# Kernel optimization log

Measured on AMD Instinct MI355X. Metric: run time of the kernel, lower is better.

## Reference

```python
import jax, jax.numpy as jnp
import numpy as np

B, S, D, H, DFF = 4, 2048, 1024, 16, 4096
DK = D // H
EPS = 1e-6


def layernorm(x, w, b):
    # Faithful to source: unbiased std (ddof=1), divides by (std + eps).
    mean = jnp.mean(x, axis=-1, keepdims=True)
    std = jnp.std(x, axis=-1, keepdims=True, ddof=1)
    return w * (x - mean) / (std + EPS) + b


def setup_inputs() -> dict:
    key = jax.random.key(0)
    ks = jax.random.split(key, 16)
    g = lambda k, shape: (jax.random.normal(k, shape, dtype=jnp.float32) * 0.02)
    inp = {
        "x": jax.random.normal(ks[0], (B, S, D), dtype=jnp.float32),
        "mask": jnp.ones((B, 1, 1, S), dtype=jnp.int32),
        # attention projections (stored [in, out]; math identical to torch Linear)
        "wq": g(ks[1], (D, D)), "bq": jnp.zeros((D,), jnp.float32),
        "wk": g(ks[2], (D, D)), "bk": jnp.zeros((D,), jnp.float32),
        "wv": g(ks[3], (D, D)), "bv": jnp.zeros((D,), jnp.float32),
        "wo": g(ks[4], (D, D)), "bo": jnp.zeros((D,), jnp.float32),
        # feed-forward
        "w1": g(ks[5], (D, DFF)), "b1": jnp.zeros((DFF,), jnp.float32),
        "w2": g(ks[6], (DFF, D)), "b2": jnp.zeros((D,), jnp.float32),
        # layer norms
        "ln1_w": jnp.ones((D,), jnp.float32), "ln1_b": jnp.zeros((D,), jnp.float32),
        "ln2_w": jnp.ones((D,), jnp.float32), "ln2_b": jnp.zeros((D,), jnp.float32),
    }
    return inp


def attention(xn, mask, wq, bq, wk, bk, wv, bv, wo, bo):
    q = (xn @ wq + bq).reshape(B, S, H, DK)
    k = (xn @ wk + bk).reshape(B, S, H, DK)
    v = (xn @ wv + bv).reshape(B, S, H, DK)
    scores = jnp.einsum("bqhd,bkhd->bhqk", q, k) / jnp.sqrt(jnp.float32(DK))
    scores = jnp.where(mask == 0, -jnp.inf, scores)
    attn = jax.nn.softmax(scores, axis=-1)  # dropout identity at inference
    out = jnp.einsum("bhqk,bkhd->bqhd", attn, v).reshape(B, S, D)
    return out @ wo + bo


def reference(x, mask, wq, bq, wk, bk, wv, bv, wo, bo,
              w1, b1, w2, b2, ln1_w, ln1_b, ln2_w, ln2_b):
    # pre-norm residual 1: self-attention
    x = x + attention(layernorm(x, ln1_w, ln1_b), mask,
                      wq, bq, wk, bk, wv, bv, wo, bo)
    # pre-norm residual 2: FFN
    xn = layernorm(x, ln2_w, ln2_b)
    ffn = jax.nn.relu(xn @ w1 + b1) @ w2 + b2
    return x + ffn
```

## Files before the change

kernel.cpp:

```cpp
#include <hip/hip_runtime.h>


typedef unsigned short u16;
typedef unsigned u32;
typedef __bf16 bf16x8 __attribute__((ext_vector_type(8)));
typedef float f32x4 __attribute__((ext_vector_type(4)));
typedef float f32x16 __attribute__((ext_vector_type(16)));

typedef __attribute__((address_space(1))) const void* as1_cvp;
typedef __attribute__((address_space(3))) void* as3_vp;

__device__ __forceinline__ void async_copy16(const void* g, void* l) {
  __builtin_amdgcn_global_load_lds((as1_cvp)g, (as3_vp)l, 16, 0, 0);
}

__device__ __forceinline__ u16 f2bf(float f) {
  unsigned u = __float_as_uint(f);
  u += 0x7fffu + ((u >> 16) & 1u);
  return (u16)(u >> 16);
}

__device__ __forceinline__ float fast_exp2(float x) {
  return __builtin_amdgcn_exp2f(x);
}

__device__ __forceinline__ u32 cvt_pk_bf16(float lo, float hi) {
  u32 d;
  asm("v_cvt_pk_bf16_f32 %0, %1, %2" : "=v"(d) : "v"(lo), "v"(hi));
  return d;
}

__device__ __forceinline__ void permlane32_swap(u32& x, u32& y) {
  asm volatile("v_permlane32_swap_b32 %0, %1" : "+v"(x), "+v"(y));
}

__global__ __launch_bounds__(256) void k_transpose_bf16(
    const float* __restrict__ src, u16* __restrict__ dst, int K, int N,
    float scale) {
  __shared__ float tile[32][33];
  int n0 = blockIdx.x * 32, k0 = blockIdx.y * 32;
  int c = threadIdx.x & 31, r0 = threadIdx.x >> 5;
#pragma unroll
  for (int i = 0; i < 32; i += 8)
    tile[r0 + i][c] = src[(size_t)(k0 + r0 + i) * N + n0 + c];
  __syncthreads();
#pragma unroll
  for (int i = 0; i < 32; i += 8)
    dst[(size_t)(n0 + r0 + i) * K + k0 + c] = f2bf(tile[c][r0 + i] * scale);
}

__global__ __launch_bounds__(256) void k_pack_bias(
    const float* __restrict__ bq, const float* __restrict__ bk,
    const float* __restrict__ bv, float* __restrict__ out, float qscale) {
  int i = blockIdx.x * 256 + threadIdx.x;
  float v;
  if (i < 1024) v = bq[i] * qscale;
  else if (i < 2048) v = bk[i - 1024];
  else v = bv[i - 2048];
  out[i] = v;
}

__global__ __launch_bounds__(256) void k_maskadd(
    const int* __restrict__ mask, float* __restrict__ madd) {
  int i = blockIdx.x * 256 + threadIdx.x;
  madd[i] = mask[i] ? 0.0f : -1e30f;
}

__global__ __launch_bounds__(256) void k_layernorm_bf16(
    const float* __restrict__ x, const float* __restrict__ w,
    const float* __restrict__ b, u16* __restrict__ out) {
  const int D = 1024;
  int row = blockIdx.x, tid = threadIdx.x;
  const float4* xr = (const float4*)(x + (size_t)row * D);
  float4 v = xr[tid];
  float s = v.x + v.y + v.z + v.w;
  float ss = v.x * v.x + v.y * v.y + v.z * v.z + v.w * v.w;
#pragma unroll
  for (int off = 1; off < 64; off <<= 1) {
    s += __shfl_xor(s, off);
    ss += __shfl_xor(ss, off);
  }
  __shared__ float rs[4], rss[4];
  int wave = tid >> 6, lane = tid & 63;
  if (lane == 0) { rs[wave] = s; rss[wave] = ss; }
  __syncthreads();
  float S_ = rs[0] + rs[1] + rs[2] + rs[3];
  float SS = rss[0] + rss[1] + rss[2] + rss[3];
  float mean = S_ * (1.0f / D);
  float var = (SS - (float)D * mean * mean) * (1.0f / (D - 1));
  float inv = 1.0f / (sqrtf(fmaxf(var, 0.0f)) + 1e-6f);
  float4 wv = ((const float4*)w)[tid], bv = ((const float4*)b)[tid];
  u16* orow = out + (size_t)row * D + tid * 4;
  orow[0] = f2bf(wv.x * (v.x - mean) * inv + bv.x);
  orow[1] = f2bf(wv.y * (v.y - mean) * inv + bv.y);
  orow[2] = f2bf(wv.z * (v.z - mean) * inv + bv.z);
  orow[3] = f2bf(wv.w * (v.w - mean) * inv + bv.w);
}

template <bool RELU, bool HAS_RES, bool OUT_BF16>
__global__ __launch_bounds__(512, 2) void k_gemm2(
    const u16* __restrict__ A, const u16* __restrict__ Bt,
    const float* __restrict__ bias, const float* __restrict__ res,
    void* __restrict__ outp, int M, int N, int K) {
  __shared__ __align__(16) u16 lds[3 * 24576];
  const int tid = threadIdx.x;
  const int lane = tid & 63, wave = tid >> 6;
  const int quad = lane >> 4, l16 = lane & 15;
  const int m0 = blockIdx.x * 256, n0 = blockIdx.y * 128;
  const int wm = (wave >> 1) * 64, wn = (wave & 1) * 64;

  const int srow = tid >> 3;
  const int schunk8 = ((tid & 7) ^ (srow & 7)) * 8;
  const u16* gA0 = A + (size_t)(m0 + srow) * K + schunk8;
  const u16* gA1 = A + (size_t)(m0 + 64 + srow) * K + schunk8;
  const u16* gA2 = A + (size_t)(m0 + 128 + srow) * K + schunk8;
  const u16* gA3 = A + (size_t)(m0 + 192 + srow) * K + schunk8;
  const u16* gB0 = Bt + (size_t)(n0 + srow) * K + schunk8;
  const u16* gB1 = Bt + (size_t)(n0 + 64 + srow) * K + schunk8;

  auto STAGE = [&](int t, int s) {
    const size_t ko = (size_t)t * 64;
    u16* sb = lds + s * 24576;
    async_copy16(gA0 + ko, sb + tid * 8);
    async_copy16(gA1 + ko, sb + 4096 + tid * 8);
    async_copy16(gA2 + ko, sb + 8192 + tid * 8);
    async_copy16(gA3 + ko, sb + 12288 + tid * 8);
    async_copy16(gB0 + ko, sb + 16384 + tid * 8);
    async_copy16(gB1 + ko, sb + 20480 + tid * 8);
  };

  f32x4 zero = {0.0f, 0.0f, 0.0f, 0.0f};
  f32x4 acc[4][4];
#pragma unroll
  for (int i = 0; i < 4; i++)
#pragma unroll
    for (int j = 0; j < 4; j++) acc[i][j] = zero;

  STAGE(0, 0);
  STAGE(1, 1);
  const int NT = K >> 6;
  for (int t = 0; t < NT; t++) {
    asm volatile("s_waitcnt vmcnt(6)" ::: "memory");
    __builtin_amdgcn_s_barrier();
    if (t + 2 < NT) STAGE(t + 2, (t + 2) % 3);
    const u16* sb = lds + (t % 3) * 24576;
    const u16* sbB = sb + 16384;
#pragma unroll
    for (int ks = 0; ks < 2; ks++) {
      bf16x8 af[4], bfr[4];
#pragma unroll
      for (int mb = 0; mb < 4; mb++) {
        int R = wm + mb * 16 + l16;
        af[mb] = *(const bf16x8*)&sb[R * 64 + (((4 * ks + quad) ^ (R & 7)) * 8)];
      }
#pragma unroll
      for (int nb = 0; nb < 4; nb++) {
        int C = wn + nb * 16 + l16;
        bfr[nb] =
            *(const bf16x8*)&sbB[C * 64 + (((4 * ks + quad) ^ (C & 7)) * 8)];
      }
#pragma unroll
      for (int mb = 0; mb < 4; mb++)
#pragma unroll
        for (int nb = 0; nb < 4; nb++)
          acc[mb][nb] = __builtin_amdgcn_mfma_f32_16x16x32_bf16(
              af[mb], bfr[nb], acc[mb][nb], 0, 0, 0);
    }
  }
#pragma unroll
  for (int mb = 0; mb < 4; mb++) {
#pragma unroll
    for (int nb = 0; nb < 4; nb++) {
      int col = n0 + wn + nb * 16 + l16;
      float bb = bias[col];
#pragma unroll
      for (int r = 0; r < 4; r++) {
        int row = m0 + wm + mb * 16 + quad * 4 + r;
        float vv = acc[mb][nb][r] + bb;
        if (HAS_RES) vv += res[(size_t)row * N + col];
        if (RELU) vv = fmaxf(vv, 0.0f);
        if (OUT_BF16) ((u16*)outp)[(size_t)row * N + col] = f2bf(vv);
        else ((float*)outp)[(size_t)row * N + col] = vv;
      }
    }
  }
}

__global__ __launch_bounds__(256, 2) void k_attention(
    const u16* __restrict__ qkv, const float* __restrict__ madd,
    u16* __restrict__ out) {
  const int S = 2048, D = 1024, QS = 3072;
  int blk = blockIdx.x;
  int xcd = blk & 7, t0 = blk >> 3;
  int qt = t0 & 7, gg = t0 >> 3;
  int g = gg * 8 + xcd;
  int h = g & 15, bb = g >> 4;
  int tid = threadIdx.x, lane = tid & 63, wave = tid >> 6;
  int l32 = lane & 31, hh = lane >> 5;

  __shared__ __align__(16) u16 Ks[64 * 64];
  __shared__ __align__(16) u16 Vs[64 * 64];
  __shared__ __align__(16) float Ms[2048];

  const int qrowbase = bb * S + qt * 256;
  const int sbase = bb * S;

  bf16x8 qf0[4], qf1[4];
  {
    const u16* qp0 =
        qkv + (size_t)(qrowbase + wave * 64 + l32) * QS + h * 64 + 8 * hh;
    const u16* qp1 = qp0 + (size_t)32 * QS;
#pragma unroll
    for (int c = 0; c < 4; c++) {
      qf0[c] = *(const bf16x8*)(qp0 + 16 * c);
      qf1[c] = *(const bf16x8*)(qp1 + 16 * c);
    }
  }

  bf16x8 ones;
  {
    union { u16 s[8]; bf16x8 v; } o_;
#pragma unroll
    for (int j = 0; j < 8; j++) o_.s[j] = 0x3F80;
    ones = o_.v;
  }

  f32x16 accA0, accB0, lacc0, accA1, accB1, lacc1;
#pragma unroll
  for (int r = 0; r < 16; r++) {
    accA0[r] = 0.0f; accB0[r] = 0.0f; lacc0[r] = 0.0f;
    accA1[r] = 0.0f; accB1[r] = 0.0f; lacc1[r] = 0.0f;
  }

  async_copy16(madd + sbase + tid * 4, (float*)Ms + tid * 4);
  async_copy16(madd + sbase + (tid + 256) * 4, (float*)Ms + (tid + 256) * 4);

#pragma unroll 1
  for (int kt = 0; kt < 32; kt++) {
    const int kb0 = sbase + kt * 64;
    __syncthreads();
#pragma unroll
    for (int s = 0; s < 2; s++) {
      int c = tid + s * 256;
      int krow = c >> 3, ko = ((c & 7) ^ (krow & 7)) * 8;
      async_copy16(qkv + (size_t)(kb0 + krow) * QS + 1024 + h * 64 + ko,
                   Ks + c * 8);
    }
#pragma unroll
    for (int s = 0; s < 2; s++) {
      int jb = tid + s * 256;
      int vkey = jb >> 3, vf = jb & 7;
      union { uint4 u; u16 s16[8]; } tt;
      tt.u = *(const uint4*)(qkv + (size_t)(kb0 + vkey) * QS + 2048 + h * 64 +
                             vf * 8);
#pragma unroll
      for (int j = 0; j < 8; j++)
        Vs[(8 * vf + j) * 64 + (vkey ^ (8 * (vf ^ j)))] = tt.s16[j];
    }
    __syncthreads();

#pragma unroll
    for (int kb = 0; kb < 2; kb++) {
      const int kr = kb * 32 + l32;
      bf16x8 kf[4];
#pragma unroll
      for (int c = 0; c < 4; c++)
        kf[c] = *(const bf16x8*)&Ks[kr * 64 + (((2 * c + hh) ^ (kr & 7)) * 8)];
      f32x16 s0, s1;
#pragma unroll
      for (int r = 0; r < 16; r++) { s0[r] = 0.0f; s1[r] = 0.0f; }
#pragma unroll
      for (int c = 0; c < 4; c++) {
        s0 = __builtin_amdgcn_mfma_f32_32x32x16_bf16(kf[c], qf0[c], s0, 0, 0, 0);
        s1 = __builtin_amdgcn_mfma_f32_32x32x16_bf16(kf[c], qf1[c], s1, 0, 0, 0);
      }
#pragma unroll
      for (int m = 0; m < 4; m++) {
        f32x4 mv = *(const f32x4*)&Ms[kt * 64 + kb * 32 + m * 8 + 4 * hh];
#pragma unroll
        for (int r = 0; r < 4; r++) {
          s0[m * 4 + r] = fast_exp2(s0[m * 4 + r] + mv[r]);
          s1[m * 4 + r] = fast_exp2(s1[m * 4 + r] + mv[r]);
        }
      }
#pragma unroll
      for (int hk = 0; hk < 2; hk++) {
        u32 a0 = cvt_pk_bf16(s0[hk * 8 + 0], s0[hk * 8 + 1]);
        u32 a1 = cvt_pk_bf16(s0[hk * 8 + 2], s0[hk * 8 + 3]);
        u32 b0 = cvt_pk_bf16(s0[hk * 8 + 4], s0[hk * 8 + 5]);
        u32 b1 = cvt_pk_bf16(s0[hk * 8 + 6], s0[hk * 8 + 7]);
        permlane32_swap(a0, b0);
        permlane32_swap(a1, b1);
        union { u32 u[4]; bf16x8 v; } p0;
        p0.u[0] = a0; p0.u[1] = a1; p0.u[2] = b0; p0.u[3] = b1;
        u32 c0 = cvt_pk_bf16(s1[hk * 8 + 0], s1[hk * 8 + 1]);
        u32 c1 = cvt_pk_bf16(s1[hk * 8 + 2], s1[hk * 8 + 3]);
        u32 d0 = cvt_pk_bf16(s1[hk * 8 + 4], s1[hk * 8 + 5]);
        u32 d1 = cvt_pk_bf16(s1[hk * 8 + 6], s1[hk * 8 + 7]);
        permlane32_swap(c0, d0);
        permlane32_swap(c1, d1);
        union { u32 u[4]; bf16x8 v; } p1;
        p1.u[0] = c0; p1.u[1] = c1; p1.u[2] = d0; p1.u[3] = d1;

        const int kc = kb * 2 + hk;
        const int kch = 2 * kc + hh;
        lacc0 = __builtin_amdgcn_mfma_f32_32x32x16_bf16(p0.v, ones, lacc0, 0, 0, 0);
        lacc1 = __builtin_amdgcn_mfma_f32_32x32x16_bf16(p1.v, ones, lacc1, 0, 0, 0);
        const int r0v = l32;
        bf16x8 v0 = *(const bf16x8*)&Vs[r0v * 64 +
                                        ((kch ^ (((r0v >> 3) ^ r0v) & 7)) * 8)];
        accA0 = __builtin_amdgcn_mfma_f32_32x32x16_bf16(p0.v, v0, accA0, 0, 0, 0);
        accA1 = __builtin_amdgcn_mfma_f32_32x32x16_bf16(p1.v, v0, accA1, 0, 0, 0);
        const int r1v = 32 + l32;
        bf16x8 v1 = *(const bf16x8*)&Vs[r1v * 64 +
                                        ((kch ^ (((r1v >> 3) ^ r1v) & 7)) * 8)];
        accB0 = __builtin_amdgcn_mfma_f32_32x32x16_bf16(p0.v, v1, accB0, 0, 0, 0);
        accB1 = __builtin_amdgcn_mfma_f32_32x32x16_bf16(p1.v, v1, accB1, 0, 0, 0);
      }
    }
  }

#pragma unroll
  for (int r = 0; r < 16; r++) {
    float i0 = 1.0f / lacc0[r];
    float i1 = 1.0f / lacc1[r];
    size_t row0 =
        (size_t)(qrowbase + wave * 64 + (r & 3) + 8 * (r >> 2) + 4 * hh);
    u16* op0 = out + row0 * D + h * 64;
    op0[l32] = f2bf(accA0[r] * i0);
    op0[32 + l32] = f2bf(accB0[r] * i0);
    u16* op1 = op0 + (size_t)32 * D;
    op1[l32] = f2bf(accA1[r] * i1);
    op1[32 + l32] = f2bf(accB1[r] * i1);
  }
}

extern "C" void kernel_launch(void* const* d_in, const int* in_sizes, int n_in,
                              void* d_out, int out_size, void* d_ws,
                              size_t ws_size, hipStream_t stream) {
  const float* x    = (const float*)d_in[0];
  const int*   mask = (const int*)d_in[1];
  const float* wq = (const float*)d_in[2];   const float* bq = (const float*)d_in[3];
  const float* wk = (const float*)d_in[4];   const float* bk = (const float*)d_in[5];
  const float* wv = (const float*)d_in[6];   const float* bv = (const float*)d_in[7];
  const float* wo = (const float*)d_in[8];   const float* bo = (const float*)d_in[9];
  const float* w1 = (const float*)d_in[10];  const float* b1 = (const float*)d_in[11];
  const float* w2 = (const float*)d_in[12];  const float* b2 = (const float*)d_in[13];
  const float* ln1w = (const float*)d_in[14]; const float* ln1b = (const float*)d_in[15];
  const float* ln2w = (const float*)d_in[16]; const float* ln2b = (const float*)d_in[17];
  float* outp = (float*)d_out;

  char* ws = (char*)d_ws;
  const size_t MB = 1024 * 1024;
  u16* wqkvT = (u16*)(ws + 0 * MB);
  u16* woT   = (u16*)(ws + 6 * MB);
  u16* w1T   = (u16*)(ws + 8 * MB);
  u16* w2T   = (u16*)(ws + 16 * MB);
  u16* xn    = (u16*)(ws + 24 * MB);
  u16* qkvb  = (u16*)(ws + 40 * MB);
  u16* hb    = (u16*)(ws + 40 * MB);
  float* bqkv = (float*)(ws + 88 * MB);
  float* madd = (float*)(ws + 88 * MB + 64 * 1024);
  float* y1  = (float*)(ws + 104 * MB);

  const float qscale = 0.125f * 1.44269504f;

  k_transpose_bf16<<<dim3(32, 32), 256, 0, stream>>>(wq, wqkvT, 1024, 1024, qscale);
  k_transpose_bf16<<<dim3(32, 32), 256, 0, stream>>>(wk, wqkvT + 1024 * 1024, 1024, 1024, 1.0f);
  k_transpose_bf16<<<dim3(32, 32), 256, 0, stream>>>(wv, wqkvT + 2048 * 1024, 1024, 1024, 1.0f);
  k_transpose_bf16<<<dim3(32, 32), 256, 0, stream>>>(wo, woT, 1024, 1024, 1.0f);
  k_transpose_bf16<<<dim3(128, 32), 256, 0, stream>>>(w1, w1T, 1024, 4096, 1.0f);
  k_transpose_bf16<<<dim3(32, 128), 256, 0, stream>>>(w2, w2T, 4096, 1024, 1.0f);
  k_pack_bias<<<12, 256, 0, stream>>>(bq, bk, bv, bqkv, qscale);
  k_maskadd<<<32, 256, 0, stream>>>(mask, madd);

  k_layernorm_bf16<<<8192, 256, 0, stream>>>(x, ln1w, ln1b, xn);

  k_gemm2<false, false, true><<<dim3(32, 24), 512, 0, stream>>>(
      xn, wqkvT, bqkv, nullptr, qkvb, 8192, 3072, 1024);

  k_attention<<<512, 256, 0, stream>>>(qkvb, madd, xn);

  dim3 go(32, 8);
  k_gemm2<false, true, false><<<go, 512, 0, stream>>>(xn, woT, bo, x, y1, 8192, 1024, 1024);

  k_layernorm_bf16<<<8192, 256, 0, stream>>>(y1, ln2w, ln2b, xn);

  k_gemm2<true, false, true><<<dim3(32, 32), 512, 0, stream>>>(
      xn, w1T, b1, nullptr, hb, 8192, 4096, 1024);

  k_gemm2<false, true, false><<<go, 512, 0, stream>>>(hb, w2T, b2, y1, outp, 8192, 1024, 4096);
}
```

Baseline: 482.6 us.

## Double-buffer K/V tiles in attention and compute row sums in registers

Adds ping-pong LDS buffers for K and V so the next tile's loads are issued before computing on the current tile, leaving one barrier per iteration instead of two. The softmax denominator is now accumulated per lane with scalar fp32 adds and combined through shared memory at the end, replacing the extra MFMA against a ones vector. This doubles LDS use for K/V and may reduce occupancy, and it adds register pressure from the prefetched V values.

```diff
diff --git a/kernel.cpp b/kernel.cpp
--- a/kernel.cpp
+++ b/kernel.cpp
@@ -198,9 +198,10 @@
   int tid = threadIdx.x, lane = tid & 63, wave = tid >> 6;
   int l32 = lane & 31, hh = lane >> 5;
 
-  __shared__ __align__(16) u16 Ks[64 * 64];
-  __shared__ __align__(16) u16 Vs[64 * 64];
+  __shared__ __align__(16) u16 Ks[2][64 * 64];
+  __shared__ __align__(16) u16 Vs[2][64 * 64];
   __shared__ __align__(16) float Ms[2048];
+  __shared__ float Dn[4][2][64];
 
   const int qrowbase = bb * S + qt * 256;
   const int sbase = bb * S;
@@ -217,47 +218,54 @@
     }
   }
 
-  bf16x8 ones;
-  {
-    union { u16 s[8]; bf16x8 v; } o_;
-#pragma unroll
-    for (int j = 0; j < 8; j++) o_.s[j] = 0x3F80;
-    ones = o_.v;
-  }
-
-  f32x16 accA0, accB0, lacc0, accA1, accB1, lacc1;
+  f32x16 accA0, accB0, accA1, accB1;
 #pragma unroll
   for (int r = 0; r < 16; r++) {
-    accA0[r] = 0.0f; accB0[r] = 0.0f; lacc0[r] = 0.0f;
-    accA1[r] = 0.0f; accB1[r] = 0.0f; lacc1[r] = 0.0f;
-  }
+    accA0[r] = 0.0f; accB0[r] = 0.0f;
+    accA1[r] = 0.0f; accB1[r] = 0.0f;
+  }
+  float dsum0 = 0.0f, dsum1 = 0.0f;
+
+  const int c0j = tid, c1j = tid + 256;
+  const int kr0 = c0j >> 3, ko0 = ((c0j & 7) ^ (kr0 & 7)) * 8;
+  const int kr1 = c1j >> 3, ko1 = ((c1j & 7) ^ (kr1 & 7)) * 8;
+  const int vk0 = c0j >> 3, vf0 = c0j & 7;
+  const int vk1 = c1j >> 3, vf1 = c1j & 7;
 
   async_copy16(madd + sbase + tid * 4, (float*)Ms + tid * 4);
   async_copy16(madd + sbase + (tid + 256) * 4, (float*)Ms + (tid + 256) * 4);
+  async_copy16(qkv + (size_t)(sbase + kr0) * QS + 1024 + h * 64 + ko0,
+               Ks[0] + c0j * 8);
+  async_copy16(qkv + (size_t)(sbase + kr1) * QS + 1024 + h * 64 + ko1,
+               Ks[0] + c1j * 8);
+  {
+    union { uint4 u; u16 s16[8]; } t0v, t1v;
+    t0v.u = *(const uint4*)(qkv + (size_t)(sbase + vk0) * QS + 2048 + h * 64 +
+                            vf0 * 8);
+    t1v.u = *(const uint4*)(qkv + (size_t)(sbase + vk1) * QS + 2048 + h * 64 +
+                            vf1 * 8);
+#pragma unroll
+    for (int j = 0; j < 8; j++) {
+      Vs[0][(8 * vf0 + j) * 64 + (vk0 ^ (8 * (vf0 ^ j)))] = t0v.s16[j];
+      Vs[0][(8 * vf1 + j) * 64 + (vk1 ^ (8 * (vf1 ^ j)))] = t1v.s16[j];
+    }
+  }
+  asm volatile("s_waitcnt vmcnt(0) lgkmcnt(0)" ::: "memory");
+  __syncthreads();
 
 #pragma unroll 1
   for (int kt = 0; kt < 32; kt++) {
-    const int kb0 = sbase + kt * 64;
-    __syncthreads();
-#pragma unroll
-    for (int s = 0; s < 2; s++) {
-      int c = tid + s * 256;
-      int krow = c >> 3, ko = ((c & 7) ^ (krow & 7)) * 8;
-      async_copy16(qkv + (size_t)(kb0 + krow) * QS + 1024 + h * 64 + ko,
-                   Ks + c * 8);
-    }
-#pragma unroll
-    for (int s = 0; s < 2; s++) {
-      int jb = tid + s * 256;
-      int vkey = jb >> 3, vf = jb & 7;
-      union { uint4 u; u16 s16[8]; } tt;
-      tt.u = *(const uint4*)(qkv + (size_t)(kb0 + vkey) * QS + 2048 + h * 64 +
-                             vf * 8);
-#pragma unroll
-      for (int j = 0; j < 8; j++)
-        Vs[(8 * vf + j) * 64 + (vkey ^ (8 * (vf ^ j)))] = tt.s16[j];
-    }
-    __syncthreads();
+    const int p = kt & 1, np = p ^ 1;
+    const int ktn = kt < 31 ? kt + 1 : 31;
+    const int nb0 = sbase + ktn * 64;
+    async_copy16(qkv + (size_t)(nb0 + kr0) * QS + 1024 + h * 64 + ko0,
+                 Ks[np] + c0j * 8);
+    async_copy16(qkv + (size_t)(nb0 + kr1) * QS + 1024 + h * 64 + ko1,
+                 Ks[np] + c1j * 8);
+    uint4 vbn0 = *(const uint4*)(qkv + (size_t)(nb0 + vk0) * QS + 2048 +
+                                 h * 64 + vf0 * 8);
+    uint4 vbn1 = *(const uint4*)(qkv + (size_t)(nb0 + vk1) * QS + 2048 +
+                                 h * 64 + vf1 * 8);
 
 #pragma unroll
     for (int kb = 0; kb < 2; kb++) {
@@ -265,7 +273,8 @@
       bf16x8 kf[4];
 #pragma unroll
       for (int c = 0; c < 4; c++)
-        kf[c] = *(const bf16x8*)&Ks[kr * 64 + (((2 * c + hh) ^ (kr & 7)) * 8)];
+        kf[c] =
+            *(const bf16x8*)&Ks[p][kr * 64 + (((2 * c + hh) ^ (kr & 7)) * 8)];
       f32x16 s0, s1;
 #pragma unroll
       for (int r = 0; r < 16; r++) { s0[r] = 0.0f; s1[r] = 0.0f; }
@@ -283,6 +292,8 @@
           s1[m * 4 + r] = fast_exp2(s1[m * 4 + r] + mv[r]);
         }
       }
+#pragma unroll
+      for (int m2 = 0; m2 < 16; m2++) { dsum0 += s0[m2]; dsum1 += s1[m2]; }
 #pragma unroll
       for (int hk = 0; hk < 2; hk++) {
         u32 a0 = cvt_pk_bf16(s0[hk * 8 + 0], s0[hk * 8 + 1]);
@@ -304,28 +315,43 @@
 
         const int kc = kb * 2 + hk;
         const int kch = 2 * kc + hh;
-        lacc0 = __builtin_amdgcn_mfma_f32_32x32x16_bf16(p0.v, ones, lacc0, 0, 0, 0);
-        lacc1 = __builtin_amdgcn_mfma_f32_32x32x16_bf16(p1.v, ones, lacc1, 0, 0, 0);
         const int r0v = l32;
-        bf16x8 v0 = *(const bf16x8*)&Vs[r0v * 64 +
-                                        ((kch ^ (((r0v >> 3) ^ r0v) & 7)) * 8)];
+        bf16x8 v0 = *(const bf16x8*)&Vs[p][r0v * 64 +
+                                          ((kch ^ (((r0v >> 3) ^ r0v) & 7)) * 8)];
         accA0 = __builtin_amdgcn_mfma_f32_32x32x16_bf16(p0.v, v0, accA0, 0, 0, 0);
         accA1 = __builtin_amdgcn_mfma_f32_32x32x16_bf16(p1.v, v0, accA1, 0, 0, 0);
         const int r1v = 32 + l32;
-        bf16x8 v1 = *(const bf16x8*)&Vs[r1v * 64 +
-                                        ((kch ^ (((r1v >> 3) ^ r1v) & 7)) * 8)];
+        bf16x8 v1 = *(const bf16x8*)&Vs[p][r1v * 64 +
+                                          ((kch ^ (((r1v >> 3) ^ r1v) & 7)) * 8)];
         accB0 = __builtin_amdgcn_mfma_f32_32x32x16_bf16(p0.v, v1, accB0, 0, 0, 0);
         accB1 = __builtin_amdgcn_mfma_f32_32x32x16_bf16(p1.v, v1, accB1, 0, 0, 0);
       }
     }
-  }
+
+    {
+      union { uint4 u; u16 s16[8]; } t0v, t1v;
+      t0v.u = vbn0;
+      t1v.u = vbn1;
+#pragma unroll
+      for (int j = 0; j < 8; j++) {
+        Vs[np][(8 * vf0 + j) * 64 + (vk0 ^ (8 * (vf0 ^ j)))] = t0v.s16[j];
+        Vs[np][(8 * vf1 + j) * 64 + (vk1 ^ (8 * (vf1 ^ j)))] = t1v.s16[j];
+      }
+    }
+    asm volatile("s_waitcnt vmcnt(0) lgkmcnt(0)" ::: "memory");
+    __builtin_amdgcn_s_barrier();
+  }
+
+  Dn[wave][0][lane] = dsum0;
+  Dn[wave][1][lane] = dsum1;
+  __syncthreads();
 
 #pragma unroll
   for (int r = 0; r < 16; r++) {
-    float i0 = 1.0f / lacc0[r];
-    float i1 = 1.0f / lacc1[r];
-    size_t row0 =
-        (size_t)(qrowbase + wave * 64 + (r & 3) + 8 * (r >> 2) + 4 * hh);
+    int q32 = (r & 3) + 8 * (r >> 2) + 4 * hh;
+    float i0 = 1.0f / (Dn[wave][0][q32] + Dn[wave][0][q32 + 32]);
+    float i1 = 1.0f / (Dn[wave][1][q32] + Dn[wave][1][q32 + 32]);
+    size_t row0 = (size_t)(qrowbase + wave * 64 + q32);
     u16* op0 = out + row0 * D + h * 64;
     op0[l32] = f2bf(accA0[r] * i0);
     op0[32 + l32] = f2bf(accB0[r] * i0);
```

New measurement: 497.4 us. 3.1% more time.
